# Kernel optimization log

Hardware: AMD Instinct MI355X
Metric: run time of the kernel (lower is better)

## Reference

```python
import jax, jax.numpy as jnp
import numpy as np

C = 256          # channels
NH = 8           # heads
DH = 64          # dim_head
NMEM = 4         # num_mem_kv
HIDDEN = NH * DH # 512
SCALE = DH ** (-0.5)


def _rmsnorm(x, gain):
    # F.normalize(x, dim=1) * gain * sqrt(C)  (scale-only RMS norm over channel dim)
    n = jnp.sqrt(jnp.sum(x * x, axis=1, keepdims=True))
    return x / jnp.maximum(n, 1e-12) * gain * (x.shape[1] ** 0.5)


def setup_inputs() -> dict:
    key = jax.random.key(0)
    ks = jax.random.split(key, 6)
    B, Hh, Ww = 16, 64, 64
    return {
        "x": jax.random.normal(ks[0], (B, C, Hh, Ww), jnp.float32),
        "gain1": jnp.ones((1, C, 1, 1), jnp.float32),
        "w_qkv": jax.random.normal(ks[1], (3 * HIDDEN, C), jnp.float32) * 0.02,
        "mem_kv": jax.random.normal(ks[2], (2, NH, DH, NMEM), jnp.float32),
        "w_out": jax.random.normal(ks[3], (C, HIDDEN), jnp.float32) * 0.02,
        "b_out": jnp.zeros((C,), jnp.float32),
        "gain2": jnp.ones((1, C, 1, 1), jnp.float32),
    }


def reference(x, gain1, w_qkv, mem_kv, w_out, b_out, gain2):
    B, _, Hh, Ww = x.shape
    N = Hh * Ww
    # pre-norm
    xn = _rmsnorm(x, gain1)
    # 1x1 conv QKV projection (no bias) == channel GEMM
    qkv = jnp.einsum('oc,bchw->bohw', w_qkv, xn)          # [B, 3*hidden, H, W]
    qkv = qkv.reshape(B, 3, NH, DH, N)                    # chunk + 'b (h c) x y -> b h c (x y)'
    q, k, v = qkv[:, 0], qkv[:, 1], qkv[:, 2]             # [B, h, d, N]
    # learned global memory kv, broadcast over batch
    mem_k = jnp.broadcast_to(mem_kv[0], (B, NH, DH, NMEM))
    mem_v = jnp.broadcast_to(mem_kv[1], (B, NH, DH, NMEM))
    k = jnp.concatenate([mem_k, k], axis=-1)              # [B, h, d, NMEM+N]
    v = jnp.concatenate([mem_v, v], axis=-1)
    # dual softmax: q over feature dim d, k over token dim n
    q = jax.nn.softmax(q, axis=-2) * SCALE
    k = jax.nn.softmax(k, axis=-1)
    # linear attention: O(N) context
    context = jnp.einsum('bhdn,bhen->bhde', k, v)         # [B, h, d, e]
    out = jnp.einsum('bhde,bhdn->bhen', context, q)       # [B, h, e, N]
    out = out.reshape(B, HIDDEN, Hh, Ww)
    # 1x1 conv out projection (with bias) + post RMSNorm
    out = jnp.einsum('oc,bchw->bohw', w_out, out) + b_out[None, :, None, None]
    return _rmsnorm(out, gain2)
```

## Files before the change

kernel.cpp:

```cpp
#include <hip/hip_runtime.h>

typedef __attribute__((ext_vector_type(8))) short bf16x8;
typedef __attribute__((ext_vector_type(4))) short bf16x4;
typedef __attribute__((ext_vector_type(4))) float f32x4;
typedef unsigned short u16;

constexpr int B_   = 16;
constexpr int C_   = 256;
constexpr int NH   = 8;
constexpr int DH   = 64;
constexpr int NMEM = 4;
constexpr int HID  = 512;
constexpr int QKVC = 1536;
constexpr int N_   = 4096;
constexpr int CTXS = 4224;

__device__ __forceinline__ u16 f2b(float f) {
  union { float f; unsigned u; } v{f};
  unsigned r = v.u + 0x7fff + ((v.u >> 16) & 1);
  return (u16)(r >> 16);
}
__device__ __forceinline__ float b2f(u16 h) {
  union { unsigned u; float f; } v; v.u = ((unsigned)h) << 16; return v.f;
}

__device__ __forceinline__ void gld_lds16(const u16* g, u16* l) {
  __builtin_amdgcn_global_load_lds(
      (const __attribute__((address_space(1))) unsigned*)g,
      (__attribute__((address_space(3))) unsigned*)l, 16, 0, 0);
}

__global__ void k_cvtw(const float* __restrict__ wq, const float* __restrict__ wo,
                       u16* __restrict__ wqb, u16* __restrict__ wob) {
  int i = blockIdx.x * 256 + threadIdx.x;
  for (int idx = i; idx < QKVC * C_; idx += gridDim.x * 256) wqb[idx] = f2b(wq[idx]);
  for (int idx = i; idx < C_ * HID; idx += gridDim.x * 256) wob[idx] = f2b(wo[idx]);
}

__global__ __launch_bounds__(256) void k_rms1(const float* __restrict__ x,
                                              const float* __restrict__ g1,
                                              u16* __restrict__ xbT) {
  int g = blockIdx.y;
  int n = blockIdx.x * 64 + (threadIdx.x & 63);
  int ch = threadIdx.x >> 6;
  __shared__ float ssp[4][64];
  __shared__ float invs[64];
  const float* xp = x + (size_t)g * C_ * N_ + n;
  float ss = 0.f;
  #pragma unroll 16
  for (int c = ch * 64; c < ch * 64 + 64; ++c) {
    float v = xp[(size_t)c * N_];
    ss += v * v;
  }
  ssp[ch][n & 63] = ss;
  __syncthreads();
  if (threadIdx.x < 64) {
    float tot = (ssp[0][threadIdx.x] + ssp[1][threadIdx.x]) +
                (ssp[2][threadIdx.x] + ssp[3][threadIdx.x]);
    invs[threadIdx.x] = 16.0f / fmaxf(sqrtf(tot), 1e-12f);
  }
  __syncthreads();
  float inv = invs[n & 63];
  u16* op = xbT + ((size_t)g * N_ + n) * C_;
  #pragma unroll 2
  for (int c0 = ch * 64; c0 < ch * 64 + 64; c0 += 8) {
    union { bf16x8 v; u16 u[8]; } pk;
    #pragma unroll
    for (int j = 0; j < 8; ++j) pk.u[j] = f2b(xp[(size_t)(c0 + j) * N_] * inv * g1[c0 + j]);
    *(bf16x8*)(op + c0) = pk.v;
  }
}

__global__ __launch_bounds__(256) void k_kvctx(const u16* __restrict__ Wb,
                                               const u16* __restrict__ XT,
                                               float* __restrict__ ctxp) {
  __shared__ __align__(16) u16 smem[16384];
  u16* Ws = smem;
  u16* Xs = smem + 8192;
  u16* Pl = smem;
  u16* Vl = smem + 8192;

  int cpx = gridDim.x >> 3;
  int bid = blockIdx.x;
  int L = (bid & 7) * cpx + (bid >> 3);
  int h = L & 7, nc = (L >> 3) & 7, g = L >> 6;
  int t = threadIdx.x, wave = t >> 6, lane = t & 63;
  int wm = wave >> 1, wn = wave & 1;
  int kg = lane >> 4, lr = lane & 15;

  const u16* WK = Wb + (size_t)(HID + h * DH) * C_;
  const u16* WV = Wb + (size_t)(2 * HID + h * DH) * C_;
  const u16* Xg = XT + ((size_t)g * N_ + nc * 512) * C_;

  int rl8 = lane >> 3;
  int cs8 = (lane & 7) ^ rl8;
  const u16* Wsrc = (wave < 2) ? WK : WV;

  f32x4 acc2[4];
  #pragma unroll
  for (int nf = 0; nf < 4; ++nf) acc2[nf] = (f32x4)0.f;
  float rs[4] = {0.f, 0.f, 0.f, 0.f};

  for (int it = 0; it < 4; ++it) {
    f32x4 acc[4][4];
    #pragma unroll
    for (int i = 0; i < 4; ++i)
      #pragma unroll
      for (int j = 0; j < 4; ++j) acc[i][j] = (f32x4)0.f;

    for (int k0 = 0; k0 < C_; k0 += 64) {
      #pragma unroll
      for (int q = 0; q < 4; ++q) {
        int rb = wave * 32 + q * 8;
        int rw = (rb & 63) + rl8;
        int rx = it * 128 + rb + rl8;
        gld_lds16(Wsrc + (size_t)rw * C_ + k0 + cs8 * 8, Ws + rb * 64);
        gld_lds16(Xg + (size_t)rx * C_ + k0 + cs8 * 8, Xs + rb * 64);
      }
      __syncthreads();
      #pragma unroll
      for (int ks = 0; ks < 2; ++ks) {
        int ch = ks * 4 + kg;
        bf16x8 a[4], bv[4];
        #pragma unroll
        for (int mf = 0; mf < 4; ++mf) {
          int r = wm * 64 + mf * 16 + lr;
          a[mf] = *(const bf16x8*)(Xs + r * 64 + ((ch ^ (r & 7)) * 8));
        }
        #pragma unroll
        for (int nf = 0; nf < 4; ++nf) {
          int r = wn * 64 + nf * 16 + lr;
          bv[nf] = *(const bf16x8*)(Ws + r * 64 + ((ch ^ (r & 7)) * 8));
        }
        #pragma unroll
        for (int mf = 0; mf < 4; ++mf)
          #pragma unroll
          for (int nf = 0; nf < 4; ++nf)
            acc[mf][nf] = __builtin_amdgcn_mfma_f32_16x16x32_bf16(a[mf], bv[nf], acc[mf][nf], 0, 0, 0);
      }
      __syncthreads();
    }

    if (wn == 0) {
      #pragma unroll
      for (int mf = 0; mf < 4; ++mf) {
        int nb = wm * 64 + mf * 16 + kg * 4;
        int cc = nb >> 3, off = nb & 7;
        #pragma unroll
        for (int nf = 0; nf < 4; ++nf) {
          int d = nf * 16 + lr;
          float e0 = __expf(acc[mf][nf][0]);
          float e1 = __expf(acc[mf][nf][1]);
          float e2 = __expf(acc[mf][nf][2]);
          float e3 = __expf(acc[mf][nf][3]);
          rs[nf] += (e0 + e1) + (e2 + e3);
          union { bf16x4 v; u16 u[4]; } pk;
          pk.u[0] = f2b(e0); pk.u[1] = f2b(e1); pk.u[2] = f2b(e2); pk.u[3] = f2b(e3);
          *(bf16x4*)(Pl + d * 128 + ((cc ^ (d & 15)) * 8) + off) = pk.v;
        }
      }
    } else {
      #pragma unroll
      for (int mf = 0; mf < 4; ++mf) {
        int nb = wm * 64 + mf * 16 + kg * 4;
        int cc = nb >> 3, off = nb & 7;
        #pragma unroll
        for (int nf = 0; nf < 4; ++nf) {
          int e = nf * 16 + lr;
          union { bf16x4 v; u16 u[4]; } pk;
          pk.u[0] = f2b(acc[mf][nf][0]); pk.u[1] = f2b(acc[mf][nf][1]);
          pk.u[2] = f2b(acc[mf][nf][2]); pk.u[3] = f2b(acc[mf][nf][3]);
          *(bf16x4*)(Vl + e * 128 + ((cc ^ (e & 15)) * 8) + off) = pk.v;
        }
      }
    }
    __syncthreads();

    #pragma unroll
    for (int k = 0; k < 4; ++k) {
      int c = k * 4 + kg;
      bf16x8 af = *(const bf16x8*)(Pl + (wave * 16 + lr) * 128 + ((c ^ lr) * 8));
      #pragma unroll
      for (int nf = 0; nf < 4; ++nf) {
        bf16x8 bfv = *(const bf16x8*)(Vl + (nf * 16 + lr) * 128 + ((c ^ lr) * 8));
        acc2[nf] = __builtin_amdgcn_mfma_f32_16x16x32_bf16(af, bfv, acc2[nf], 0, 0, 0);
      }
    }
    __syncthreads();
  }

  float* cgp = ctxp + ((size_t)(g * NH + h) * 8 + nc) * CTXS;
  #pragma unroll
  for (int nf = 0; nf < 4; ++nf)
    #pragma unroll
    for (int j = 0; j < 4; ++j) {
      int d = wave * 16 + kg * 4 + j;
      int e = nf * 16 + lr;
      cgp[d * 64 + e] = acc2[nf][j];
    }
  if (wn == 0) {
    #pragma unroll
    for (int nf = 0; nf < 4; ++nf) {
      rs[nf] += __shfl_xor(rs[nf], 16);
      rs[nf] += __shfl_xor(rs[nf], 32);
    }
    if (lane < 16) {
      #pragma unroll
      for (int nf = 0; nf < 4; ++nf)
        cgp[4096 + wm * 64 + nf * 16 + lane] = rs[nf];
    }
  }
}

__global__ __launch_bounds__(256) void k_cwo(const float* __restrict__ ctxp,
                                             const float* __restrict__ memkv,
                                             const u16* __restrict__ Wo,
                                             u16* __restrict__ wo2) {
  int g = blockIdx.y, h = blockIdx.x;
  int t = threadIdx.x, wave = t >> 6, lane = t & 63;
  int kg = lane >> 4, lr = lane & 15;
  int rl8 = lane >> 3, cs8 = (lane & 7) ^ rl8;
  __shared__ float emk[DH * NMEM];
  __shared__ float sd[DH];
  __shared__ __align__(16) u16 Cl[64 * 64];
  __shared__ __align__(16) u16 As2[256 * 64];

  const float* mk = memkv + (size_t)h * DH * NMEM;
  const float* mv = memkv + (size_t)(NH + h) * DH * NMEM;
  const float* cp = ctxp + (size_t)(g * NH + h) * 8 * CTXS;
  emk[t] = __expf(mk[t]);
  __syncthreads();
  if (t < DH) {
    float s = 0.f;
    #pragma unroll
    for (int p = 0; p < 8; ++p)
      s += cp[p * CTXS + 4096 + t] + cp[p * CTXS + 4160 + t];
    #pragma unroll
    for (int j = 0; j < NMEM; ++j) s += emk[t * 4 + j];
    sd[t] = s;
  }
  #pragma unroll
  for (int q = 0; q < 8; ++q) {
    int rb = wave * 64 + q * 8;
    gld_lds16(Wo + (size_t)(rb + rl8) * HID + h * DH + cs8 * 8, As2 + rb * 64);
  }
  __syncthreads();
  #pragma unroll
  for (int i = 0; i < 16; ++i) {
    int idx = t + 256 * i;
    int d = idx >> 6, e = idx & 63;
    float v = 0.f;
    #pragma unroll
    for (int p = 0; p < 8; ++p) v += cp[p * CTXS + idx];
    #pragma unroll
    for (int j = 0; j < NMEM; ++j) v += emk[d * 4 + j] * mv[e * 4 + j];
    Cl[d * 64 + (((e >> 3) ^ (d & 7)) * 8) + (e & 7)] = f2b(v / sd[d]);
  }
  __syncthreads();
  f32x4 acc[4][4];
  #pragma unroll
  for (int i = 0; i < 4; ++i)
    #pragma unroll
    for (int j = 0; j < 4; ++j) acc[i][j] = (f32x4)0.f;
  #pragma unroll
  for (int ks = 0; ks < 2; ++ks) {
    int ch = ks * 4 + kg;
    bf16x8 a[4], b[4];
    #pragma unroll
    for (int mf = 0; mf < 4; ++mf) {
      int r = wave * 64 + mf * 16 + lr;
      a[mf] = *(const bf16x8*)(As2 + r * 64 + ((ch ^ (r & 7)) * 8));
    }
    #pragma unroll
    for (int nf = 0; nf < 4; ++nf) {
      int rd = nf * 16 + lr;
      b[nf] = *(const bf16x8*)(Cl + rd * 64 + ((ch ^ (rd & 7)) * 8));
    }
    #pragma unroll
    for (int mf = 0; mf < 4; ++mf)
      #pragma unroll
      for (int nf = 0; nf < 4; ++nf)
        acc[mf][nf] = __builtin_amdgcn_mfma_f32_16x16x32_bf16(a[mf], b[nf], acc[mf][nf], 0, 0, 0);
  }
  u16* og = wo2 + (size_t)g * 256 * 512;
  #pragma unroll
  for (int mf = 0; mf < 4; ++mf)
    #pragma unroll
    for (int nf = 0; nf < 4; ++nf)
      #pragma unroll
      for (int j = 0; j < 4; ++j) {
        int c = wave * 64 + mf * 16 + kg * 4 + j;
        int dd = nf * 16 + lr;
        og[(size_t)c * 512 + h * DH + dd] = f2b(acc[mf][nf][j]);
      }
}

__global__ __launch_bounds__(1024) void k_qout(const u16* __restrict__ Wq,
                                               const u16* __restrict__ XT,
                                               const u16* __restrict__ Wo2,
                                               const float* __restrict__ bias,
                                               const float* __restrict__ g2,
                                               float* __restrict__ out) {
  __shared__ __align__(16) u16 smem[49152];
  u16* R0 = smem;
  u16* R1 = smem + 16384;

  int cpx = gridDim.x >> 3;
  int bid = blockIdx.x;
  int L = (bid & 7) * cpx + (bid >> 3);
  int nc = L & 31, g = L >> 5;
  int t = threadIdx.x, wave = t >> 6, lane = t & 63;
  int kg = lane >> 4, lr = lane & 15;
  int rl4 = lane >> 2, cs4 = (lane & 3) ^ (rl4 & 3);
  int rl8 = lane >> 3, cs8 = (lane & 7) ^ rl8;
  int hq = wave & 7, nh2 = wave >> 3;

  const u16* Xg = XT + ((size_t)g * N_ + nc * 128) * C_;
  const u16* W2g = Wo2 + (size_t)g * 256 * 512;

  {
    int xrow_off = lane >> 5;
    int c32 = lane & 31;
    #pragma unroll
    for (int q = 0; q < 4; ++q) {
      int base = wave * 8 + q * 2;
      int row = base + xrow_off;
      int sw = (c32 & 24) | ((c32 & 7) ^ (row & 7));
      gld_lds16(Xg + (size_t)row * C_ + sw * 8, R1 + base * 256);
    }
  }

  f32x4 acc[4][4];
  #pragma unroll
  for (int i = 0; i < 4; ++i)
    #pragma unroll
    for (int j = 0; j < 4; ++j) acc[i][j] = (f32x4)0.f;

  for (int k0i = 0; k0i < 8; ++k0i) {
    int k0 = k0i * 32;
    #pragma unroll
    for (int q = 0; q < 2; ++q) {
      int rb = ((wave * 2 + q) & 31) * 16;
      gld_lds16(Wq + (size_t)(rb + rl4) * C_ + k0 + cs4 * 8, R0 + rb * 32);
    }
    __syncthreads();
    bf16x8 a[4], bv[4];
    #pragma unroll
    for (int mf = 0; mf < 4; ++mf) {
      int r = hq * 64 + mf * 16 + lr;
      a[mf] = *(const bf16x8*)(R0 + r * 32 + ((kg ^ (r & 3)) * 8));
    }
    #pragma unroll
    for (int nf = 0; nf < 4; ++nf) {
      int bn = nh2 * 64 + nf * 16 + lr;
      int c32 = k0i * 4 + kg;
      int sw = (c32 & 24) | ((c32 & 7) ^ (bn & 7));
      bv[nf] = *(const bf16x8*)(R1 + bn * 256 + sw * 8);
    }
    #pragma unroll
    for (int mf = 0; mf < 4; ++mf)
      #pragma unroll
      for (int nf = 0; nf < 4; ++nf)
        acc[mf][nf] = __builtin_amdgcn_mfma_f32_16x16x32_bf16(a[mf], bv[nf], acc[mf][nf], 0, 0, 0);
    __syncthreads();
  }

  float colsum[4];
  #pragma unroll
  for (int nf = 0; nf < 4; ++nf) {
    float s = 0.f;
    #pragma unroll
    for (int mf = 0; mf < 4; ++mf)
      #pragma unroll
      for (int j = 0; j < 4; ++j) {
        float e = __expf(acc[mf][nf][j]);
        acc[mf][nf][j] = e;
        s += e;
      }
    colsum[nf] = s;
  }
  #pragma unroll
  for (int nf = 0; nf < 4; ++nf) {
    colsum[nf] += __shfl_xor(colsum[nf], 16);
    colsum[nf] += __shfl_xor(colsum[nf], 32);
    colsum[nf] = 0.125f / colsum[nf];
  }
  unsigned pq[4][4][2];
  #pragma unroll
  for (int nf = 0; nf < 4; ++nf) {
    float invs = colsum[nf];
    #pragma unroll
    for (int mf = 0; mf < 4; ++mf)
      #pragma unroll
      for (int jp = 0; jp < 2; ++jp) {
        u16 lo = f2b(acc[mf][nf][jp * 2] * invs);
        u16 hi = f2b(acc[mf][nf][jp * 2 + 1] * invs);
        pq[mf][nf][jp] = (unsigned)lo | ((unsigned)hi << 16);
      }
  }

  int wc = wave & 7;
  f32x4 acc2[2][4];
  #pragma unroll
  for (int i = 0; i < 2; ++i)
    #pragma unroll
    for (int j = 0; j < 4; ++j) acc2[i][j] = (f32x4)0.f;

  #pragma unroll
  for (int half = 0; half < 2; ++half) {
    if ((hq >> 2) == half) {
      #pragma unroll
      for (int nf = 0; nf < 4; ++nf) {
        int n = nh2 * 64 + nf * 16 + lr;
        #pragma unroll
        for (int mf = 0; mf < 4; ++mf)
          #pragma unroll
          for (int jp = 0; jp < 2; ++jp) {
            int oc = (hq & 3) * 64 + mf * 16 + kg * 4 + jp * 2;
            int c8 = oc >> 3;
            int sw = (c8 & 24) | ((c8 & 7) ^ (n & 7));
            *(unsigned*)(R1 + n * 256 + sw * 8 + (oc & 7)) = pq[mf][nf][jp];
          }
      }
    }
    __syncthreads();
    for (int k0l = 0; k0l < 4; ++k0l) {
      int cb = half * 256 + k0l * 64;
      #pragma unroll
      for (int q = 0; q < 2; ++q) {
        int rb = ((wave * 2 + q) & 31) * 8;
        gld_lds16(W2g + (size_t)(rb + rl8) * 512 + cb + cs8 * 8, R0 + rb * 64);
      }
      __syncthreads();
      #pragma unroll
      for (int ks = 0; ks < 2; ++ks) {
        int ch = ks * 4 + kg;
        bf16x8 a2[2], b2[4];
        #pragma unroll
        for (int mf = 0; mf < 2; ++mf) {
          int r = wc * 32 + mf * 16 + lr;
          a2[mf] = *(const bf16x8*)(R0 + r * 64 + ((ch ^ (r & 7)) * 8));
        }
        #pragma unroll
        for (int nf = 0; nf < 4; ++nf) {
          int bn = nh2 * 64 + nf * 16 + lr;
          int c8 = k0l * 8 + ks * 4 + kg;
          int sw = (c8 & 24) | ((c8 & 7) ^ (bn & 7));
          b2[nf] = *(const bf16x8*)(R1 + bn * 256 + sw * 8);
        }
        #pragma unroll
        for (int mf = 0; mf < 2; ++mf)
          #pragma unroll
          for (int nf = 0; nf < 4; ++nf)
            acc2[mf][nf] = __builtin_amdgcn_mfma_f32_16x16x32_bf16(a2[mf], b2[nf], acc2[mf][nf], 0, 0, 0);
      }
      __syncthreads();
    }
  }

  float colsq[4] = {0.f, 0.f, 0.f, 0.f};
  #pragma unroll
  for (int mf = 0; mf < 2; ++mf)
    #pragma unroll
    for (int j = 0; j < 4; ++j) {
      int c = wc * 32 + mf * 16 + kg * 4 + j;
      float bs = bias[c];
      #pragma unroll
      for (int nf = 0; nf < 4; ++nf) {
        float v = acc2[mf][nf][j] + bs;
        acc2[mf][nf][j] = v;
        colsq[nf] += v * v;
      }
    }
  #pragma unroll
  for (int nf = 0; nf < 4; ++nf) {
    colsq[nf] += __shfl_xor(colsq[nf], 16);
    colsq[nf] += __shfl_xor(colsq[nf], 32);
  }
  float* part = (float*)R0;
  if (kg == 0) {
    #pragma unroll
    for (int nf = 0; nf < 4; ++nf) part[wave * 64 + nf * 16 + lr] = colsq[nf];
  }
  __syncthreads();
  float* og = out + (size_t)g * C_ * N_ + nc * 128;
  #pragma unroll
  for (int nf = 0; nf < 4; ++nf) {
    int cl_ = nf * 16 + lr;
    float tot = 0.f;
    #pragma unroll
    for (int w = 0; w < 8; ++w) tot += part[(nh2 * 8 + w) * 64 + cl_];
    float invn = 16.0f / fmaxf(sqrtf(tot), 1e-12f);
    int col = nh2 * 64 + cl_;
    #pragma unroll
    for (int mf = 0; mf < 2; ++mf)
      #pragma unroll
      for (int j = 0; j < 4; ++j) {
        int c = wc * 32 + mf * 16 + kg * 4 + j;
        og[(size_t)c * N_ + col] = acc2[mf][nf][j] * invn * g2[c];
      }
  }
}

extern "C" void kernel_launch(void* const* d_in, const int* in_sizes, int n_in,
                              void* d_out, int out_size, void* d_ws, size_t ws_size,
                              hipStream_t stream) {
  (void)in_sizes; (void)n_in; (void)out_size;
  const float* x      = (const float*)d_in[0];
  const float* gain1  = (const float*)d_in[1];
  const float* w_qkv  = (const float*)d_in[2];
  const float* mem_kv = (const float*)d_in[3];
  const float* w_out  = (const float*)d_in[4];
  const float* b_out  = (const float*)d_in[5];
  const float* gain2  = (const float*)d_in[6];
  float* out = (float*)d_out;

  char* ws = (char*)d_ws;
  u16* wqkvb = (u16*)ws;
  u16* woutb = (u16*)(ws + 786432);
  size_t shared_b = 1048576;

  const size_t xbT_b  = (size_t)N_ * C_ * 2;
  const size_t ctxp_b = (size_t)NH * 8 * CTXS * 4;
  const size_t wo2_b  = (size_t)256 * 512 * 2;
  const size_t per_b  = xbT_b + ctxp_b + wo2_b;

  int G = 16;
  while (G > 1 && shared_b + (size_t)G * per_b > ws_size) G >>= 1;

  char* base = ws + shared_b;
  u16*   xbT  = (u16*)base;
  float* ctxp = (float*)(base + (size_t)G * xbT_b);
  u16*   wo2  = (u16*)(base + (size_t)G * (xbT_b + ctxp_b));

  k_cvtw<<<256, 256, 0, stream>>>(w_qkv, w_out, wqkvb, woutb);

  for (int b0 = 0; b0 < B_; b0 += G) {
    const float* xc = x + (size_t)b0 * C_ * N_;
    float*       oc = out + (size_t)b0 * C_ * N_;
    k_rms1  <<<dim3(N_ / 64, G),   256, 0, stream>>>(xc, gain1, xbT);
    k_kvctx <<<dim3(64 * G),       256, 0, stream>>>(wqkvb, xbT, ctxp);
    k_cwo   <<<dim3(NH, G),        256, 0, stream>>>(ctxp, mem_kv, woutb, wo2);
    k_qout  <<<dim3(32 * G),       1024, 0, stream>>>(wqkvb, xbT, wo2, b_out, gain2, oc);
  }
}
```

Baseline: 161.9 us.

## Register-prefetch weight tiles and use LDS-only barriers in fused q/out kernel

Weight tiles for the Q projection and the output projection are now loaded into registers one step ahead, then stored to swizzled LDS, instead of being loaded directly to LDS by global_load_lds and waited on at each barrier. Barriers are replaced with inline s_barrier that waits only on lgkmcnt, so the prefetched global loads can stay in flight across the barrier. This aims to hide global-memory latency behind MFMA work. It costs extra VGPRs in a 1024-thread block, adds LDS store instructions, and relies on the compiler inserting the vmcnt wait before each register use.

```diff
diff --git a/kernel.cpp b/kernel.cpp
--- a/kernel.cpp
+++ b/kernel.cpp
@@ -14,6 +14,9 @@
 constexpr int QKVC = 1536;
 constexpr int N_   = 4096;
 constexpr int CTXS = 4224;
+
+#define SBAR() asm volatile("s_waitcnt lgkmcnt(0)\ns_barrier" ::: "memory")
+#define KBAR() asm volatile("s_waitcnt vmcnt(0) lgkmcnt(0)\ns_barrier" ::: "memory")
 
 __device__ __forceinline__ u16 f2b(float f) {
   union { float f; unsigned u; } v{f};
@@ -311,8 +314,8 @@
   int nc = L & 31, g = L >> 5;
   int t = threadIdx.x, wave = t >> 6, lane = t & 63;
   int kg = lane >> 4, lr = lane & 15;
-  int rl4 = lane >> 2, cs4 = (lane & 3) ^ (rl4 & 3);
-  int rl8 = lane >> 3, cs8 = (lane & 7) ^ rl8;
+  int rl4 = lane >> 2, ch4 = lane & 3;
+  int rl8 = lane >> 3, ch8 = lane & 7;
   int hq = wave & 7, nh2 = wave >> 3;
 
   const u16* Xg = XT + ((size_t)g * N_ + nc * 128) * C_;
@@ -329,6 +332,13 @@
       gld_lds16(Xg + (size_t)row * C_ + sw * 8, R1 + base * 256);
     }
   }
+  bf16x8 wreg[2], wo2reg[2];
+  #pragma unroll
+  for (int q = 0; q < 2; ++q) {
+    int row = ((wave * 2 + q) & 31) * 16 + rl4;
+    wreg[q] = *(const bf16x8*)(Wq + (size_t)row * C_ + ch4 * 8);
+  }
+  KBAR();
 
   f32x4 acc[4][4];
   #pragma unroll
@@ -336,14 +346,27 @@
     #pragma unroll
     for (int j = 0; j < 4; ++j) acc[i][j] = (f32x4)0.f;
 
+  #pragma unroll
   for (int k0i = 0; k0i < 8; ++k0i) {
-    int k0 = k0i * 32;
     #pragma unroll
     for (int q = 0; q < 2; ++q) {
-      int rb = ((wave * 2 + q) & 31) * 16;
-      gld_lds16(Wq + (size_t)(rb + rl4) * C_ + k0 + cs4 * 8, R0 + rb * 32);
-    }
-    __syncthreads();
+      int row = ((wave * 2 + q) & 31) * 16 + rl4;
+      *(bf16x8*)(R0 + row * 32 + ((ch4 ^ (row & 3)) * 8)) = wreg[q];
+    }
+    if (k0i < 7) {
+      #pragma unroll
+      for (int q = 0; q < 2; ++q) {
+        int row = ((wave * 2 + q) & 31) * 16 + rl4;
+        wreg[q] = *(const bf16x8*)(Wq + (size_t)row * C_ + (k0i + 1) * 32 + ch4 * 8);
+      }
+    } else {
+      #pragma unroll
+      for (int q = 0; q < 2; ++q) {
+        int row = ((wave * 2 + q) & 31) * 8 + rl8;
+        wo2reg[q] = *(const bf16x8*)(W2g + (size_t)row * 512 + ch8 * 8);
+      }
+    }
+    SBAR();
     bf16x8 a[4], bv[4];
     #pragma unroll
     for (int mf = 0; mf < 4; ++mf) {
@@ -362,7 +385,7 @@
       #pragma unroll
       for (int nf = 0; nf < 4; ++nf)
         acc[mf][nf] = __builtin_amdgcn_mfma_f32_16x16x32_bf16(a[mf], bv[nf], acc[mf][nf], 0, 0, 0);
-    __syncthreads();
+    SBAR();
   }
 
   float colsum[4];
@@ -408,6 +431,7 @@
 
   #pragma unroll
   for (int half = 0; half < 2; ++half) {
+    SBAR();
     if ((hq >> 2) == half) {
       #pragma unroll
       for (int nf = 0; nf < 4; ++nf) {
@@ -423,15 +447,23 @@
           }
       }
     }
-    __syncthreads();
+    SBAR();
+    #pragma unroll
     for (int k0l = 0; k0l < 4; ++k0l) {
-      int cb = half * 256 + k0l * 64;
       #pragma unroll
       for (int q = 0; q < 2; ++q) {
-        int rb = ((wave * 2 + q) & 31) * 8;
-        gld_lds16(W2g + (size_t)(rb + rl8) * 512 + cb + cs8 * 8, R0 + rb * 64);
-      }
-      __syncthreads();
+        int row = ((wave * 2 + q) & 31) * 8 + rl8;
+        *(bf16x8*)(R0 + row * 64 + ((ch8 ^ (row & 7)) * 8)) = wo2reg[q];
+      }
+      if (half * 4 + k0l < 7) {
+        int cbn = (half * 4 + k0l + 1) * 64;
+        #pragma unroll
+        for (int q = 0; q < 2; ++q) {
+          int row = ((wave * 2 + q) & 31) * 8 + rl8;
+          wo2reg[q] = *(const bf16x8*)(W2g + (size_t)row * 512 + cbn + ch8 * 8);
+        }
+      }
+      SBAR();
       #pragma unroll
       for (int ks = 0; ks < 2; ++ks) {
         int ch = ks * 4 + kg;
@@ -454,7 +486,7 @@
           for (int nf = 0; nf < 4; ++nf)
             acc2[mf][nf] = __builtin_amdgcn_mfma_f32_16x16x32_bf16(a2[mf], b2[nf], acc2[mf][nf], 0, 0, 0);
       }
-      __syncthreads();
+      SBAR();
     }
   }
 
```

New measurement: 162.0 us. No clear change (+0.0%).
